# Optimization experiments

Hardware: AMD Instinct MI355X
Metric: run time of the kernel (lower is better)

Reference implementation:

```python
import jax, jax.numpy as jnp
import numpy as np

EMB = 1024
HEADS = 16
HEAD_DIM = EMB // HEADS


def setup_inputs() -> dict:
    key = jax.random.key(0)
    ks = jax.random.split(key, 9)
    B, T = 2, 2048
    s = 1.0 / np.sqrt(EMB)
    x = jax.random.normal(ks[0], (B, T, EMB), dtype=jnp.float32)
    Wq = jax.random.normal(ks[1], (EMB, EMB), dtype=jnp.float32) * s
    bq = jnp.zeros((EMB,), dtype=jnp.float32)
    Wk = jax.random.normal(ks[2], (EMB, EMB), dtype=jnp.float32) * s
    bk = jnp.zeros((EMB,), dtype=jnp.float32)
    Wv = jax.random.normal(ks[3], (EMB, EMB), dtype=jnp.float32) * s
    bv = jnp.zeros((EMB,), dtype=jnp.float32)
    Wo = jax.random.normal(ks[4], (EMB, EMB), dtype=jnp.float32) * s
    bo = jnp.zeros((EMB,), dtype=jnp.float32)
    return {"x": x, "Wq": Wq, "bq": bq, "Wk": Wk, "bk": bk,
            "Wv": Wv, "bv": bv, "Wo": Wo, "bo": bo}


def reference(x, Wq, bq, Wk, bk, Wv, bv, Wo, bo):
    B, T, C = x.shape
    H, D = HEADS, HEAD_DIM
    # QKV projections -> (B, H, T, D)
    q = (x @ Wq + bq).reshape(B, T, H, D).transpose(0, 2, 1, 3)
    k = (x @ Wk + bk).reshape(B, T, H, D).transpose(0, 2, 1, 3)
    v = (x @ Wv + bv).reshape(B, T, H, D).transpose(0, 2, 1, 3)
    scores = jnp.einsum('bhqd,bhkd->bhqk', q, k) / np.sqrt(D).astype(np.float32)
    causal = jnp.tril(jnp.ones((T, T), dtype=bool))  # True where allowed
    scores = jnp.where(causal, scores, -jnp.inf)
    weights = jax.nn.softmax(scores, axis=-1)  # dropout is identity at eval
    out = jnp.einsum('bhqk,bhkd->bhqd', weights, v)
    out = out.transpose(0, 2, 1, 3).reshape(B, T, C)
    return out @ Wo + bo
```

## Files before the change

kernel.cpp:

```cpp
#include <hip/hip_runtime.h>

typedef unsigned short u16;
typedef u16 u16x8 __attribute__((ext_vector_type(8)));
typedef __bf16 bf16x8 __attribute__((ext_vector_type(8)));
typedef float f32x4 __attribute__((ext_vector_type(4)));

#define EMB 1024
#define TT 2048
#define BB 2
#define NHEADS 16
#define HD 64
#define MTOT (BB * TT)

__device__ __forceinline__ u16 f2bf(float f) {
  unsigned u = __builtin_bit_cast(unsigned, f);
  u += 0x7fffu + ((u >> 16) & 1u);
  return (u16)(u >> 16);
}

__device__ __forceinline__ bf16x8 asbf(u16x8 v) {
  return __builtin_bit_cast(bf16x8, v);
}

__device__ __forceinline__ void gload16(const void* g, void* l) {
  __builtin_amdgcn_global_load_lds(
      (const __attribute__((address_space(1))) void*)g,
      (__attribute__((address_space(3))) void*)l, 16, 0, 0);
}

__global__ __launch_bounds__(256) void k_conv_x(const float* __restrict__ x,
                                                u16* __restrict__ xb) {
  int i = blockIdx.x * 256 + threadIdx.x;
  float4 a = ((const float4*)x)[i * 2];
  float4 b = ((const float4*)x)[i * 2 + 1];
  u16x8 o;
  o[0] = f2bf(a.x); o[1] = f2bf(a.y); o[2] = f2bf(a.z); o[3] = f2bf(a.w);
  o[4] = f2bf(b.x); o[5] = f2bf(b.y); o[6] = f2bf(b.z); o[7] = f2bf(b.w);
  ((u16x8*)xb)[i] = o;
}

__global__ __launch_bounds__(256) void k_conv_wT4(
    const float* __restrict__ W0, const float* __restrict__ W1,
    const float* __restrict__ W2, const float* __restrict__ W3,
    u16* __restrict__ T0, u16* __restrict__ T1, u16* __restrict__ T2,
    u16* __restrict__ T3) {
  const int z = blockIdx.z;
  const float* __restrict__ W = (z == 0) ? W0 : (z == 1) ? W1 : (z == 2) ? W2 : W3;
  u16* __restrict__ Wt = (z == 0) ? T0 : (z == 1) ? T1 : (z == 2) ? T2 : T3;
  __shared__ float tile[32][33];
  int bx = blockIdx.x * 32, by = blockIdx.y * 32;
  int tx = threadIdx.x & 31;
  int ty = threadIdx.x >> 5;
#pragma unroll
  for (int r = ty; r < 32; r += 8) tile[r][tx] = W[(by + r) * EMB + bx + tx];
  __syncthreads();
#pragma unroll
  for (int r = ty; r < 32; r += 8)
    Wt[(bx + r) * EMB + by + tx] = f2bf(tile[tx][r]);
}

__global__ __launch_bounds__(256) void k_gemm_qkv(
    const u16* __restrict__ xb, const u16* __restrict__ WqT,
    const u16* __restrict__ WkT, const u16* __restrict__ WvT,
    const float* __restrict__ bq, const float* __restrict__ bk,
    const float* __restrict__ bv, u16* __restrict__ Q, u16* __restrict__ K,
    u16* __restrict__ Vt) {
  __shared__ u16 Al[128 * 32];
  __shared__ u16 Bl[128 * 32];
  const int tid = threadIdx.x;
  const int lane = tid & 63;
  const int w = tid >> 6;
  const int wr = w >> 1, wc = w & 1;
  const int lr = lane & 15, lg = lane >> 4;
  const int m0 = blockIdx.x * 128;
  const int nb = blockIdx.y;
  const int seg = nb >> 3;
  const int n0 = (nb & 7) * 128;
  const u16* __restrict__ Bt = (seg == 0) ? WqT : (seg == 1) ? WkT : WvT;
  const float* __restrict__ bias = (seg == 0) ? bq : (seg == 1) ? bk : bv;

  f32x4 acc[4][4];
#pragma unroll
  for (int i = 0; i < 4; i++)
#pragma unroll
    for (int j = 0; j < 4; j++) acc[i][j] = (f32x4){0.f, 0.f, 0.f, 0.f};

  const int srow = tid >> 2;
  const int scol = (tid & 3) * 8;
  const u16* ga0 = xb + (m0 + srow) * EMB + scol;
  const u16* gb0 = Bt + (n0 + srow) * EMB + scol;
  char* la0 = (char*)Al + w * 1024;
  char* lb0 = (char*)Bl + w * 1024;

  for (int k0 = 0; k0 < EMB; k0 += 32) {
    gload16(ga0 + k0, la0);
    gload16(ga0 + 64 * EMB + k0, la0 + 4096);
    gload16(gb0 + k0, lb0);
    gload16(gb0 + 64 * EMB + k0, lb0 + 4096);
    __syncthreads();
    u16x8 af[4], bfr[4];
#pragma unroll
    for (int mi = 0; mi < 4; mi++)
      af[mi] = *(const u16x8*)&Al[(wr * 64 + mi * 16 + lr) * 32 + lg * 8];
#pragma unroll
    for (int ni = 0; ni < 4; ni++)
      bfr[ni] = *(const u16x8*)&Bl[(wc * 64 + ni * 16 + lr) * 32 + lg * 8];
#pragma unroll
    for (int mi = 0; mi < 4; mi++)
#pragma unroll
      for (int ni = 0; ni < 4; ni++)
        acc[mi][ni] = __builtin_amdgcn_mfma_f32_16x16x32_bf16(
            asbf(af[mi]), asbf(bfr[ni]), acc[mi][ni], 0, 0, 0);
    __syncthreads();
  }

#pragma unroll
  for (int mi = 0; mi < 4; mi++) {
    const int lmb = wr * 64 + mi * 16 + lg * 4;
#pragma unroll
    for (int ni = 0; ni < 4; ni++) {
      const int ln = wc * 64 + ni * 16 + lr;
      const int n = n0 + ln;
      const float bv_ = bias[n];
      const int h = n >> 6, d = n & 63;
#pragma unroll
      for (int r = 0; r < 4; r++) {
        const int m = m0 + lmb + r;
        const int b = m >> 11, t = m & 2047;
        float v = acc[mi][ni][r] + bv_;
        if (seg == 0) {
          v *= 0.125f;
          Q[(((b * NHEADS + h) * TT) + t) * HD + d] = f2bf(v);
        } else if (seg == 1) {
          K[(((b * NHEADS + h) * TT) + t) * HD + d] = f2bf(v);
        } else {
          Vt[(((b * NHEADS + h) * HD) + d) * TT + t] = f2bf(v);
        }
      }
    }
  }
}

__global__ __launch_bounds__(512) void k_attn(const u16* __restrict__ Q,
                                              const u16* __restrict__ Kg,
                                              const u16* __restrict__ Vt,
                                              u16* __restrict__ AO) {
  __shared__ u16 Kl[2][64 * 64];
  __shared__ u16 Vl[2][64 * 64];
  __shared__ u16 Plds[8][16][68];
  const int tid = threadIdx.x;
  const int lane = tid & 63;
  const int w = tid >> 6;
  const int lr = lane & 15, lg = lane >> 4;
  const int bh = blockIdx.x;
  const int pair = blockIdx.y;
  const int lo = pair, hi = 31 - pair;
  const int qblk = (w < 4) ? hi : lo;
  const int myend = qblk;
  const int q0 = qblk * 64 + (w & 3) * 16;
  const u16* __restrict__ Qh = Q + bh * TT * HD;
  const u16* __restrict__ Kh = Kg + bh * TT * HD;
  const u16* __restrict__ Vh = Vt + bh * HD * TT;

  const int srow = tid >> 3;
  const int sc = (tid & 7) ^ (srow & 7);

  u16x8 qf[2];
  qf[0] = *(const u16x8*)&Qh[(q0 + lr) * HD + lg * 8];
  qf[1] = *(const u16x8*)&Qh[(q0 + lr) * HD + 32 + lg * 8];

  f32x4 accO[4];
#pragma unroll
  for (int i = 0; i < 4; i++) accO[i] = (f32x4){0.f, 0.f, 0.f, 0.f};
  float mst[4] = {-__builtin_inff(), -__builtin_inff(), -__builtin_inff(),
                  -__builtin_inff()};
  float lsum[4] = {0.f, 0.f, 0.f, 0.f};

  const int nkt = hi + 1;

  gload16(Kh + srow * HD + sc * 8, (char*)Kl[0] + w * 1024);
  gload16(Vh + srow * TT + 0 + sc * 8, (char*)Vl[0] + w * 1024);
  __syncthreads();

  for (int kt = 0; kt < nkt; ++kt) {
    const int k0 = kt * 64;
    const int cur = kt & 1;
    if (kt + 1 < nkt) {
      const int kn = k0 + 64;
      gload16(Kh + (kn + srow) * HD + sc * 8, (char*)Kl[cur ^ 1] + w * 1024);
      gload16(Vh + srow * TT + kn + sc * 8, (char*)Vl[cur ^ 1] + w * 1024);
    }
    if (kt <= myend) {
      const char* Kc = (const char*)Kl[cur];
      const char* Vc = (const char*)Vl[cur];

      f32x4 s[4];
#pragma unroll
      for (int n = 0; n < 4; n++) s[n] = (f32x4){0.f, 0.f, 0.f, 0.f};
      __builtin_amdgcn_s_setprio(1);
#pragma unroll
      for (int n = 0; n < 4; n++) {
        const int row = n * 16 + lr;
#pragma unroll
        for (int dh = 0; dh < 2; dh++) {
          const int bo = (dh * 64 + lg * 16) ^ ((row & 7) << 4);
          u16x8 kf = *(const u16x8*)(Kc + row * 128 + bo);
          s[n] = __builtin_amdgcn_mfma_f32_16x16x32_bf16(asbf(qf[dh]),
                                                         asbf(kf), s[n], 0, 0, 0);
        }
      }
      __builtin_amdgcn_s_setprio(0);
      if (kt == myend) {
#pragma unroll
        for (int n = 0; n < 4; n++)
#pragma unroll
          for (int r = 0; r < 4; r++) {
            int col = k0 + n * 16 + lr, row = q0 + lg * 4 + r;
            if (col > row) s[n][r] = -__builtin_inff();
          }
      }
      float lmax[4];
#pragma unroll
      for (int r = 0; r < 4; r++)
        lmax[r] = fmaxf(fmaxf(s[0][r], s[1][r]), fmaxf(s[2][r], s[3][r]));
      float g0 = fmaxf(lmax[0] - mst[0], lmax[1] - mst[1]);
      float g1 = fmaxf(lmax[2] - mst[2], lmax[3] - mst[3]);
      if (!__all(fmaxf(g0, g1) <= 8.0f)) {
#pragma unroll
        for (int r = 0; r < 4; r++) {
          float rm = lmax[r];
          rm = fmaxf(rm, __shfl_xor(rm, 1, 16));
          rm = fmaxf(rm, __shfl_xor(rm, 2, 16));
          rm = fmaxf(rm, __shfl_xor(rm, 4, 16));
          rm = fmaxf(rm, __shfl_xor(rm, 8, 16));
          float mnew = fmaxf(mst[r], rm);
          float corr = __expf(mst[r] - mnew);
          lsum[r] *= corr;
          mst[r] = mnew;
#pragma unroll
          for (int dt = 0; dt < 4; dt++) accO[dt][r] *= corr;
        }
      }
#pragma unroll
      for (int r = 0; r < 4; r++) {
        float p0 = __expf(s[0][r] - mst[r]);
        float p1 = __expf(s[1][r] - mst[r]);
        float p2 = __expf(s[2][r] - mst[r]);
        float p3 = __expf(s[3][r] - mst[r]);
        lsum[r] += (p0 + p1) + (p2 + p3);
        const int row = lg * 4 + r;
        Plds[w][row][lr] = f2bf(p0);
        Plds[w][row][16 + lr] = f2bf(p1);
        Plds[w][row][32 + lr] = f2bf(p2);
        Plds[w][row][48 + lr] = f2bf(p3);
      }
      u16x8 pa0 = *(const u16x8*)&Plds[w][lr][lg * 8];
      u16x8 pa1 = *(const u16x8*)&Plds[w][lr][32 + lg * 8];
      __builtin_amdgcn_s_setprio(1);
#pragma unroll
      for (int dt = 0; dt < 4; dt++) {
        const int row = dt * 16 + lr;
        const int bo0 = (lg * 16) ^ ((row & 7) << 4);
        const int bo1 = (64 + lg * 16) ^ ((row & 7) << 4);
        u16x8 vf0 = *(const u16x8*)(Vc + row * 128 + bo0);
        u16x8 vf1 = *(const u16x8*)(Vc + row * 128 + bo1);
        accO[dt] = __builtin_amdgcn_mfma_f32_16x16x32_bf16(asbf(pa0),
                                                           asbf(vf0), accO[dt], 0, 0, 0);
        accO[dt] = __builtin_amdgcn_mfma_f32_16x16x32_bf16(asbf(pa1),
                                                           asbf(vf1), accO[dt], 0, 0, 0);
      }
      __builtin_amdgcn_s_setprio(0);
    }
    __syncthreads();
  }
  float rinv[4];
#pragma unroll
  for (int r = 0; r < 4; r++) {
    float t = lsum[r];
    t += __shfl_xor(t, 1, 16);
    t += __shfl_xor(t, 2, 16);
    t += __shfl_xor(t, 4, 16);
    t += __shfl_xor(t, 8, 16);
    rinv[r] = 1.0f / t;
  }
  const int b = bh >> 4, h = bh & 15;
#pragma unroll
  for (int dt = 0; dt < 4; dt++)
#pragma unroll
    for (int r = 0; r < 4; r++) {
      const int row = q0 + lg * 4 + r;
      const int d = h * 64 + dt * 16 + lr;
      AO[(b * TT + row) * EMB + d] = f2bf(accO[dt][r] * rinv[r]);
    }
}

__global__ __launch_bounds__(256) void k_gemm_out(const u16* __restrict__ AO,
                                                  const u16* __restrict__ WoT,
                                                  const float* __restrict__ bo,
                                                  float* __restrict__ out) {
  __shared__ u16 Al[128 * 32];
  __shared__ u16 Bl[128 * 32];
  const int tid = threadIdx.x;
  const int lane = tid & 63;
  const int w = tid >> 6;
  const int wr = w >> 1, wc = w & 1;
  const int lr = lane & 15, lg = lane >> 4;
  const int m0 = blockIdx.x * 128;
  const int n0 = blockIdx.y * 128;

  f32x4 acc[4][4];
#pragma unroll
  for (int i = 0; i < 4; i++)
#pragma unroll
    for (int j = 0; j < 4; j++) acc[i][j] = (f32x4){0.f, 0.f, 0.f, 0.f};

  const int srow = tid >> 2;
  const int scol = (tid & 3) * 8;
  const u16* ga0 = AO + (m0 + srow) * EMB + scol;
  const u16* gb0 = WoT + (n0 + srow) * EMB + scol;
  char* la0 = (char*)Al + w * 1024;
  char* lb0 = (char*)Bl + w * 1024;

  for (int k0 = 0; k0 < EMB; k0 += 32) {
    gload16(ga0 + k0, la0);
    gload16(ga0 + 64 * EMB + k0, la0 + 4096);
    gload16(gb0 + k0, lb0);
    gload16(gb0 + 64 * EMB + k0, lb0 + 4096);
    __syncthreads();
    u16x8 af[4], bfr[4];
#pragma unroll
    for (int mi = 0; mi < 4; mi++)
      af[mi] = *(const u16x8*)&Al[(wr * 64 + mi * 16 + lr) * 32 + lg * 8];
#pragma unroll
    for (int ni = 0; ni < 4; ni++)
      bfr[ni] = *(const u16x8*)&Bl[(wc * 64 + ni * 16 + lr) * 32 + lg * 8];
#pragma unroll
    for (int mi = 0; mi < 4; mi++)
#pragma unroll
      for (int ni = 0; ni < 4; ni++)
        acc[mi][ni] = __builtin_amdgcn_mfma_f32_16x16x32_bf16(
            asbf(af[mi]), asbf(bfr[ni]), acc[mi][ni], 0, 0, 0);
    __syncthreads();
  }

#pragma unroll
  for (int mi = 0; mi < 4; mi++) {
    const int lmb = wr * 64 + mi * 16 + lg * 4;
#pragma unroll
    for (int ni = 0; ni < 4; ni++) {
      const int ln = wc * 64 + ni * 16 + lr;
      const int n = n0 + ln;
      const float bv_ = bo[n];
#pragma unroll
      for (int r = 0; r < 4; r++) {
        const int m = m0 + lmb + r;
        out[m * EMB + n] = acc[mi][ni][r] + bv_;
      }
    }
  }
}

extern "C" void kernel_launch(void* const* d_in, const int* in_sizes, int n_in,
                              void* d_out, int out_size, void* d_ws,
                              size_t ws_size, hipStream_t stream) {
  const float* x = (const float*)d_in[0];
  const float* Wq = (const float*)d_in[1];
  const float* bq = (const float*)d_in[2];
  const float* Wk = (const float*)d_in[3];
  const float* bk = (const float*)d_in[4];
  const float* Wv = (const float*)d_in[5];
  const float* bv = (const float*)d_in[6];
  const float* Wo = (const float*)d_in[7];
  const float* bo = (const float*)d_in[8];
  float* out = (float*)d_out;

  char* ws = (char*)d_ws;
  u16* xb = (u16*)ws;
  u16* WqT = (u16*)(ws + (8u << 20));
  u16* WkT = (u16*)(ws + (10u << 20));
  u16* WvT = (u16*)(ws + (12u << 20));
  u16* WoT = (u16*)(ws + (14u << 20));
  u16* Qb = (u16*)(ws + (16u << 20));
  u16* Kb = (u16*)(ws + (24u << 20));
  u16* Vtb = (u16*)(ws + (32u << 20));
  u16* AO = xb;

  k_conv_x<<<2048, 256, 0, stream>>>(x, xb);
  dim3 tg(32, 32, 4);
  k_conv_wT4<<<tg, 256, 0, stream>>>(Wq, Wk, Wv, Wo, WqT, WkT, WvT, WoT);
  k_gemm_qkv<<<dim3(32, 24), 256, 0, stream>>>(xb, WqT, WkT, WvT, bq, bk, bv,
                                               Qb, Kb, Vtb);
  k_attn<<<dim3(32, 16), 512, 0, stream>>>(Qb, Kb, Vtb, AO);
  k_gemm_out<<<dim3(32, 8), 256, 0, stream>>>(AO, WoT, bo, out);
}
```

Measured before the change: 122.5 us.

## Double attention KV tile to 128, use exp2 softmax, fuse prep kernels

The attention kernel now processes 128 keys per tile instead of 64, which halves the number of loop iterations and barriers. The pipelining and causal masking are adjusted to the new tile size, and the V tile is split into two 64-wide P·V passes. Q is pre-scaled by log2(e)/8 so the softmax can use exp2f in place of __expf, and the lazy-rescale threshold is raised to match. The x conversion and weight-transpose kernels are merged into one launch, and the manual bf16 rounding is replaced by the hardware conversion. The larger tiles increase LDS and register use, and more wasted work is done on the diagonal tile.

```diff
diff --git a/kernel.cpp b/kernel.cpp
--- a/kernel.cpp
+++ b/kernel.cpp
@@ -12,10 +12,8 @@
 #define HD 64
 #define MTOT (BB * TT)
 
-__device__ __forceinline__ u16 f2bf(float f) {
-  unsigned u = __builtin_bit_cast(unsigned, f);
-  u += 0x7fffu + ((u >> 16) & 1u);
-  return (u16)(u >> 16);
+__device__ __forceinline__ u16 cvt(float f) {
+  return __builtin_bit_cast(u16, (__bf16)f);
 }
 
 __device__ __forceinline__ bf16x8 asbf(u16x8 v) {
@@ -28,35 +26,38 @@
       (__attribute__((address_space(3))) void*)l, 16, 0, 0);
 }
 
-__global__ __launch_bounds__(256) void k_conv_x(const float* __restrict__ x,
-                                                u16* __restrict__ xb) {
-  int i = blockIdx.x * 256 + threadIdx.x;
-  float4 a = ((const float4*)x)[i * 2];
-  float4 b = ((const float4*)x)[i * 2 + 1];
-  u16x8 o;
-  o[0] = f2bf(a.x); o[1] = f2bf(a.y); o[2] = f2bf(a.z); o[3] = f2bf(a.w);
-  o[4] = f2bf(b.x); o[5] = f2bf(b.y); o[6] = f2bf(b.z); o[7] = f2bf(b.w);
-  ((u16x8*)xb)[i] = o;
-}
-
-__global__ __launch_bounds__(256) void k_conv_wT4(
+__global__ __launch_bounds__(256) void k_prep(
+    const float* __restrict__ x, u16* __restrict__ xb,
     const float* __restrict__ W0, const float* __restrict__ W1,
     const float* __restrict__ W2, const float* __restrict__ W3,
     u16* __restrict__ T0, u16* __restrict__ T1, u16* __restrict__ T2,
     u16* __restrict__ T3) {
-  const int z = blockIdx.z;
+  __shared__ float tile[32][33];
+  const int bid = blockIdx.x;
+  const int tid = threadIdx.x;
+  if (bid >= 4096) {
+    int i = (bid - 4096) * 256 + tid;
+    float4 a = ((const float4*)x)[i * 2];
+    float4 b = ((const float4*)x)[i * 2 + 1];
+    u16x8 o;
+    o[0] = cvt(a.x); o[1] = cvt(a.y); o[2] = cvt(a.z); o[3] = cvt(a.w);
+    o[4] = cvt(b.x); o[5] = cvt(b.y); o[6] = cvt(b.z); o[7] = cvt(b.w);
+    ((u16x8*)xb)[i] = o;
+    return;
+  }
+  const int z = bid >> 10;
   const float* __restrict__ W = (z == 0) ? W0 : (z == 1) ? W1 : (z == 2) ? W2 : W3;
   u16* __restrict__ Wt = (z == 0) ? T0 : (z == 1) ? T1 : (z == 2) ? T2 : T3;
-  __shared__ float tile[32][33];
-  int bx = blockIdx.x * 32, by = blockIdx.y * 32;
-  int tx = threadIdx.x & 31;
-  int ty = threadIdx.x >> 5;
+  const int b = bid & 1023;
+  const int bx = (b & 31) * 32, by = (b >> 5) * 32;
+  const int tx = tid & 31;
+  const int ty = tid >> 5;
 #pragma unroll
   for (int r = ty; r < 32; r += 8) tile[r][tx] = W[(by + r) * EMB + bx + tx];
   __syncthreads();
 #pragma unroll
   for (int r = ty; r < 32; r += 8)
-    Wt[(bx + r) * EMB + by + tx] = f2bf(tile[tx][r]);
+    Wt[(bx + r) * EMB + by + tx] = cvt(tile[tx][r]);
 }
 
 __global__ __launch_bounds__(256) void k_gemm_qkv(
@@ -129,12 +130,12 @@
         const int b = m >> 11, t = m & 2047;
         float v = acc[mi][ni][r] + bv_;
         if (seg == 0) {
-          v *= 0.125f;
-          Q[(((b * NHEADS + h) * TT) + t) * HD + d] = f2bf(v);
+          v *= 0.18033688011f;
+          Q[(((b * NHEADS + h) * TT) + t) * HD + d] = cvt(v);
         } else if (seg == 1) {
-          K[(((b * NHEADS + h) * TT) + t) * HD + d] = f2bf(v);
+          K[(((b * NHEADS + h) * TT) + t) * HD + d] = cvt(v);
         } else {
-          Vt[(((b * NHEADS + h) * HD) + d) * TT + t] = f2bf(v);
+          Vt[(((b * NHEADS + h) * HD) + d) * TT + t] = cvt(v);
         }
       }
     }
@@ -145,8 +146,8 @@
                                               const u16* __restrict__ Kg,
                                               const u16* __restrict__ Vt,
                                               u16* __restrict__ AO) {
-  __shared__ u16 Kl[2][64 * 64];
-  __shared__ u16 Vl[2][64 * 64];
+  __shared__ u16 Kl[2][128 * 64];
+  __shared__ u16 Vl[2][64 * 128];
   __shared__ u16 Plds[8][16][68];
   const int tid = threadIdx.x;
   const int lane = tid & 63;
@@ -156,14 +157,16 @@
   const int pair = blockIdx.y;
   const int lo = pair, hi = 31 - pair;
   const int qblk = (w < 4) ? hi : lo;
-  const int myend = qblk;
+  const int myend = qblk >> 1;
   const int q0 = qblk * 64 + (w & 3) * 16;
   const u16* __restrict__ Qh = Q + bh * TT * HD;
   const u16* __restrict__ Kh = Kg + bh * TT * HD;
   const u16* __restrict__ Vh = Vt + bh * HD * TT;
 
-  const int srow = tid >> 3;
-  const int sc = (tid & 7) ^ (srow & 7);
+  const int krow = tid >> 3;
+  const int ksc = (tid & 7) ^ (krow & 7);
+  const int vrow = tid >> 4;
+  const int vgc = (tid & 15) ^ (vrow & 7);
 
   u16x8 qf[2];
   qf[0] = *(const u16x8*)&Qh[(q0 + lr) * HD + lg * 8];
@@ -176,34 +179,44 @@
                   -__builtin_inff()};
   float lsum[4] = {0.f, 0.f, 0.f, 0.f};
 
-  const int nkt = hi + 1;
-
-  gload16(Kh + srow * HD + sc * 8, (char*)Kl[0] + w * 1024);
-  gload16(Vh + srow * TT + 0 + sc * 8, (char*)Vl[0] + w * 1024);
+  const int nkt = (hi >> 1) + 1;
+
+#pragma unroll
+  for (int h = 0; h < 2; h++) {
+    gload16(Kh + (h * 64 + krow) * HD + ksc * 8,
+            (char*)Kl[0] + h * 8192 + w * 1024);
+    gload16(Vh + (h * 32 + vrow) * TT + 0 + vgc * 8,
+            (char*)Vl[0] + h * 8192 + w * 1024);
+  }
   __syncthreads();
 
   for (int kt = 0; kt < nkt; ++kt) {
-    const int k0 = kt * 64;
+    const int k0 = kt * 128;
     const int cur = kt & 1;
     if (kt + 1 < nkt) {
-      const int kn = k0 + 64;
-      gload16(Kh + (kn + srow) * HD + sc * 8, (char*)Kl[cur ^ 1] + w * 1024);
-      gload16(Vh + srow * TT + kn + sc * 8, (char*)Vl[cur ^ 1] + w * 1024);
+      const int kn = k0 + 128;
+#pragma unroll
+      for (int h = 0; h < 2; h++) {
+        gload16(Kh + (kn + h * 64 + krow) * HD + ksc * 8,
+                (char*)Kl[cur ^ 1] + h * 8192 + w * 1024);
+        gload16(Vh + (h * 32 + vrow) * TT + kn + vgc * 8,
+                (char*)Vl[cur ^ 1] + h * 8192 + w * 1024);
+      }
     }
     if (kt <= myend) {
       const char* Kc = (const char*)Kl[cur];
       const char* Vc = (const char*)Vl[cur];
 
-      f32x4 s[4];
-#pragma unroll
-      for (int n = 0; n < 4; n++) s[n] = (f32x4){0.f, 0.f, 0.f, 0.f};
+      f32x4 s[8];
+#pragma unroll
+      for (int n = 0; n < 8; n++) s[n] = (f32x4){0.f, 0.f, 0.f, 0.f};
       __builtin_amdgcn_s_setprio(1);
 #pragma unroll
-      for (int n = 0; n < 4; n++) {
+      for (int n = 0; n < 8; n++) {
         const int row = n * 16 + lr;
 #pragma unroll
         for (int dh = 0; dh < 2; dh++) {
-          const int bo = (dh * 64 + lg * 16) ^ ((row & 7) << 4);
+          const int bo = ((dh * 4 + lg) ^ (lr & 7)) * 16;
           u16x8 kf = *(const u16x8*)(Kc + row * 128 + bo);
           s[n] = __builtin_amdgcn_mfma_f32_16x16x32_bf16(asbf(qf[dh]),
                                                          asbf(kf), s[n], 0, 0, 0);
@@ -212,7 +225,7 @@
       __builtin_amdgcn_s_setprio(0);
       if (kt == myend) {
 #pragma unroll
-        for (int n = 0; n < 4; n++)
+        for (int n = 0; n < 8; n++)
 #pragma unroll
           for (int r = 0; r < 4; r++) {
             int col = k0 + n * 16 + lr, row = q0 + lg * 4 + r;
@@ -221,11 +234,14 @@
       }
       float lmax[4];
 #pragma unroll
-      for (int r = 0; r < 4; r++)
-        lmax[r] = fmaxf(fmaxf(s[0][r], s[1][r]), fmaxf(s[2][r], s[3][r]));
+      for (int r = 0; r < 4; r++) {
+        float a = fmaxf(fmaxf(s[0][r], s[1][r]), fmaxf(s[2][r], s[3][r]));
+        float b = fmaxf(fmaxf(s[4][r], s[5][r]), fmaxf(s[6][r], s[7][r]));
+        lmax[r] = fmaxf(a, b);
+      }
       float g0 = fmaxf(lmax[0] - mst[0], lmax[1] - mst[1]);
       float g1 = fmaxf(lmax[2] - mst[2], lmax[3] - mst[3]);
-      if (!__all(fmaxf(g0, g1) <= 8.0f)) {
+      if (!__all(fmaxf(g0, g1) <= 11.0f)) {
 #pragma unroll
         for (int r = 0; r < 4; r++) {
           float rm = lmax[r];
@@ -234,7 +250,7 @@
           rm = fmaxf(rm, __shfl_xor(rm, 4, 16));
           rm = fmaxf(rm, __shfl_xor(rm, 8, 16));
           float mnew = fmaxf(mst[r], rm);
-          float corr = __expf(mst[r] - mnew);
+          float corr = exp2f(mst[r] - mnew);
           lsum[r] *= corr;
           mst[r] = mnew;
 #pragma unroll
@@ -242,34 +258,37 @@
         }
       }
 #pragma unroll
-      for (int r = 0; r < 4; r++) {
-        float p0 = __expf(s[0][r] - mst[r]);
-        float p1 = __expf(s[1][r] - mst[r]);
-        float p2 = __expf(s[2][r] - mst[r]);
-        float p3 = __expf(s[3][r] - mst[r]);
-        lsum[r] += (p0 + p1) + (p2 + p3);
-        const int row = lg * 4 + r;
-        Plds[w][row][lr] = f2bf(p0);
-        Plds[w][row][16 + lr] = f2bf(p1);
-        Plds[w][row][32 + lr] = f2bf(p2);
-        Plds[w][row][48 + lr] = f2bf(p3);
-      }
-      u16x8 pa0 = *(const u16x8*)&Plds[w][lr][lg * 8];
-      u16x8 pa1 = *(const u16x8*)&Plds[w][lr][32 + lg * 8];
-      __builtin_amdgcn_s_setprio(1);
-#pragma unroll
-      for (int dt = 0; dt < 4; dt++) {
-        const int row = dt * 16 + lr;
-        const int bo0 = (lg * 16) ^ ((row & 7) << 4);
-        const int bo1 = (64 + lg * 16) ^ ((row & 7) << 4);
-        u16x8 vf0 = *(const u16x8*)(Vc + row * 128 + bo0);
-        u16x8 vf1 = *(const u16x8*)(Vc + row * 128 + bo1);
-        accO[dt] = __builtin_amdgcn_mfma_f32_16x16x32_bf16(asbf(pa0),
-                                                           asbf(vf0), accO[dt], 0, 0, 0);
-        accO[dt] = __builtin_amdgcn_mfma_f32_16x16x32_bf16(asbf(pa1),
-                                                           asbf(vf1), accO[dt], 0, 0, 0);
-      }
-      __builtin_amdgcn_s_setprio(0);
+      for (int p64 = 0; p64 < 2; p64++) {
+#pragma unroll
+        for (int r = 0; r < 4; r++) {
+          float p0 = exp2f(s[p64 * 4 + 0][r] - mst[r]);
+          float p1 = exp2f(s[p64 * 4 + 1][r] - mst[r]);
+          float p2 = exp2f(s[p64 * 4 + 2][r] - mst[r]);
+          float p3 = exp2f(s[p64 * 4 + 3][r] - mst[r]);
+          lsum[r] += (p0 + p1) + (p2 + p3);
+          const int row = lg * 4 + r;
+          Plds[w][row][lr] = cvt(p0);
+          Plds[w][row][16 + lr] = cvt(p1);
+          Plds[w][row][32 + lr] = cvt(p2);
+          Plds[w][row][48 + lr] = cvt(p3);
+        }
+        u16x8 pa0 = *(const u16x8*)&Plds[w][lr][lg * 8];
+        u16x8 pa1 = *(const u16x8*)&Plds[w][lr][32 + lg * 8];
+        __builtin_amdgcn_s_setprio(1);
+#pragma unroll
+        for (int dt = 0; dt < 4; dt++) {
+          const int row = dt * 16 + lr;
+          const int bo0 = p64 * 128 + ((lg ^ (lr & 7)) * 16);
+          const int bo1 = p64 * 128 + (((4 + lg) ^ (lr & 7)) * 16);
+          u16x8 vf0 = *(const u16x8*)(Vc + row * 256 + bo0);
+          u16x8 vf1 = *(const u16x8*)(Vc + row * 256 + bo1);
+          accO[dt] = __builtin_amdgcn_mfma_f32_16x16x32_bf16(
+              asbf(pa0), asbf(vf0), accO[dt], 0, 0, 0);
+          accO[dt] = __builtin_amdgcn_mfma_f32_16x16x32_bf16(
+              asbf(pa1), asbf(vf1), accO[dt], 0, 0, 0);
+        }
+        __builtin_amdgcn_s_setprio(0);
+      }
     }
     __syncthreads();
   }
@@ -290,7 +309,7 @@
     for (int r = 0; r < 4; r++) {
       const int row = q0 + lg * 4 + r;
       const int d = h * 64 + dt * 16 + lr;
-      AO[(b * TT + row) * EMB + d] = f2bf(accO[dt][r] * rinv[r]);
+      AO[(b * TT + row) * EMB + d] = cvt(accO[dt][r] * rinv[r]);
     }
 }
 
@@ -385,9 +404,7 @@
   u16* Vtb = (u16*)(ws + (32u << 20));
   u16* AO = xb;
 
-  k_conv_x<<<2048, 256, 0, stream>>>(x, xb);
-  dim3 tg(32, 32, 4);
-  k_conv_wT4<<<tg, 256, 0, stream>>>(Wq, Wk, Wv, Wo, WqT, WkT, WvT, WoT);
+  k_prep<<<6144, 256, 0, stream>>>(x, xb, Wq, Wk, Wv, Wo, WqT, WkT, WvT, WoT);
   k_gemm_qkv<<<dim3(32, 24), 256, 0, stream>>>(xb, WqT, WkT, WvT, bq, bk, bv,
                                                Qb, Kb, Vtb);
   k_attn<<<dim3(32, 16), 512, 0, stream>>>(Qb, Kb, Vtb, AO);
```

After: 136.7 us. +11.6%, slower.

## Fuse prep kernels, swizzle GEMM tiles, use exp2 softmax and hardware bf16 cvt

Applied to the files above, without the earlier changes.

Merges the x conversion and the weight transpose into a single prep launch to save one kernel launch. Remaps GEMM workgroup IDs with an XCD-style swizzle so that neighbouring tiles share cache. Folds log2(e) into the Q scale so softmax can use exp2f directly, and raises the lazy-rescale threshold to 11, which is about 8 in natural-log units. Replaces the manual round-to-nearest bf16 conversion with the compiler's native conversion.

```diff
diff --git a/kernel.cpp b/kernel.cpp
--- a/kernel.cpp
+++ b/kernel.cpp
@@ -12,10 +12,8 @@
 #define HD 64
 #define MTOT (BB * TT)
 
-__device__ __forceinline__ u16 f2bf(float f) {
-  unsigned u = __builtin_bit_cast(unsigned, f);
-  u += 0x7fffu + ((u >> 16) & 1u);
-  return (u16)(u >> 16);
+__device__ __forceinline__ u16 cvt(float f) {
+  return __builtin_bit_cast(u16, (__bf16)f);
 }
 
 __device__ __forceinline__ bf16x8 asbf(u16x8 v) {
@@ -28,35 +26,38 @@
       (__attribute__((address_space(3))) void*)l, 16, 0, 0);
 }
 
-__global__ __launch_bounds__(256) void k_conv_x(const float* __restrict__ x,
-                                                u16* __restrict__ xb) {
-  int i = blockIdx.x * 256 + threadIdx.x;
-  float4 a = ((const float4*)x)[i * 2];
-  float4 b = ((const float4*)x)[i * 2 + 1];
-  u16x8 o;
-  o[0] = f2bf(a.x); o[1] = f2bf(a.y); o[2] = f2bf(a.z); o[3] = f2bf(a.w);
-  o[4] = f2bf(b.x); o[5] = f2bf(b.y); o[6] = f2bf(b.z); o[7] = f2bf(b.w);
-  ((u16x8*)xb)[i] = o;
-}
-
-__global__ __launch_bounds__(256) void k_conv_wT4(
+__global__ __launch_bounds__(256) void k_prep(
+    const float* __restrict__ x, u16* __restrict__ xb,
     const float* __restrict__ W0, const float* __restrict__ W1,
     const float* __restrict__ W2, const float* __restrict__ W3,
     u16* __restrict__ T0, u16* __restrict__ T1, u16* __restrict__ T2,
     u16* __restrict__ T3) {
-  const int z = blockIdx.z;
+  __shared__ float tile[32][33];
+  const int bid = blockIdx.x;
+  const int tid = threadIdx.x;
+  if (bid >= 4096) {
+    int i = (bid - 4096) * 256 + tid;
+    float4 a = ((const float4*)x)[i * 2];
+    float4 b = ((const float4*)x)[i * 2 + 1];
+    u16x8 o;
+    o[0] = cvt(a.x); o[1] = cvt(a.y); o[2] = cvt(a.z); o[3] = cvt(a.w);
+    o[4] = cvt(b.x); o[5] = cvt(b.y); o[6] = cvt(b.z); o[7] = cvt(b.w);
+    ((u16x8*)xb)[i] = o;
+    return;
+  }
+  const int z = bid >> 10;
   const float* __restrict__ W = (z == 0) ? W0 : (z == 1) ? W1 : (z == 2) ? W2 : W3;
   u16* __restrict__ Wt = (z == 0) ? T0 : (z == 1) ? T1 : (z == 2) ? T2 : T3;
-  __shared__ float tile[32][33];
-  int bx = blockIdx.x * 32, by = blockIdx.y * 32;
-  int tx = threadIdx.x & 31;
-  int ty = threadIdx.x >> 5;
+  const int b = bid & 1023;
+  const int bx = (b & 31) * 32, by = (b >> 5) * 32;
+  const int tx = tid & 31;
+  const int ty = tid >> 5;
 #pragma unroll
   for (int r = ty; r < 32; r += 8) tile[r][tx] = W[(by + r) * EMB + bx + tx];
   __syncthreads();
 #pragma unroll
   for (int r = ty; r < 32; r += 8)
-    Wt[(bx + r) * EMB + by + tx] = f2bf(tile[tx][r]);
+    Wt[(bx + r) * EMB + by + tx] = cvt(tile[tx][r]);
 }
 
 __global__ __launch_bounds__(256) void k_gemm_qkv(
@@ -72,8 +73,10 @@
   const int w = tid >> 6;
   const int wr = w >> 1, wc = w & 1;
   const int lr = lane & 15, lg = lane >> 4;
-  const int m0 = blockIdx.x * 128;
-  const int nb = blockIdx.y;
+  const int wg = blockIdx.y * 32 + blockIdx.x;
+  const int swz = (wg & 7) * 96 + (wg >> 3);
+  const int m0 = (swz & 31) * 128;
+  const int nb = swz >> 5;
   const int seg = nb >> 3;
   const int n0 = (nb & 7) * 128;
   const u16* __restrict__ Bt = (seg == 0) ? WqT : (seg == 1) ? WkT : WvT;
@@ -129,12 +132,12 @@
         const int b = m >> 11, t = m & 2047;
         float v = acc[mi][ni][r] + bv_;
         if (seg == 0) {
-          v *= 0.125f;
-          Q[(((b * NHEADS + h) * TT) + t) * HD + d] = f2bf(v);
+          v *= 0.18033688011f;
+          Q[(((b * NHEADS + h) * TT) + t) * HD + d] = cvt(v);
         } else if (seg == 1) {
-          K[(((b * NHEADS + h) * TT) + t) * HD + d] = f2bf(v);
+          K[(((b * NHEADS + h) * TT) + t) * HD + d] = cvt(v);
         } else {
-          Vt[(((b * NHEADS + h) * HD) + d) * TT + t] = f2bf(v);
+          Vt[(((b * NHEADS + h) * HD) + d) * TT + t] = cvt(v);
         }
       }
     }
@@ -225,7 +228,7 @@
         lmax[r] = fmaxf(fmaxf(s[0][r], s[1][r]), fmaxf(s[2][r], s[3][r]));
       float g0 = fmaxf(lmax[0] - mst[0], lmax[1] - mst[1]);
       float g1 = fmaxf(lmax[2] - mst[2], lmax[3] - mst[3]);
-      if (!__all(fmaxf(g0, g1) <= 8.0f)) {
+      if (!__all(fmaxf(g0, g1) <= 11.0f)) {
 #pragma unroll
         for (int r = 0; r < 4; r++) {
           float rm = lmax[r];
@@ -234,7 +237,7 @@
           rm = fmaxf(rm, __shfl_xor(rm, 4, 16));
           rm = fmaxf(rm, __shfl_xor(rm, 8, 16));
           float mnew = fmaxf(mst[r], rm);
-          float corr = __expf(mst[r] - mnew);
+          float corr = exp2f(mst[r] - mnew);
           lsum[r] *= corr;
           mst[r] = mnew;
 #pragma unroll
@@ -243,16 +246,16 @@
       }
 #pragma unroll
       for (int r = 0; r < 4; r++) {
-        float p0 = __expf(s[0][r] - mst[r]);
-        float p1 = __expf(s[1][r] - mst[r]);
-        float p2 = __expf(s[2][r] - mst[r]);
-        float p3 = __expf(s[3][r] - mst[r]);
+        float p0 = exp2f(s[0][r] - mst[r]);
+        float p1 = exp2f(s[1][r] - mst[r]);
+        float p2 = exp2f(s[2][r] - mst[r]);
+        float p3 = exp2f(s[3][r] - mst[r]);
         lsum[r] += (p0 + p1) + (p2 + p3);
         const int row = lg * 4 + r;
-        Plds[w][row][lr] = f2bf(p0);
-        Plds[w][row][16 + lr] = f2bf(p1);
-        Plds[w][row][32 + lr] = f2bf(p2);
-        Plds[w][row][48 + lr] = f2bf(p3);
+        Plds[w][row][lr] = cvt(p0);
+        Plds[w][row][16 + lr] = cvt(p1);
+        Plds[w][row][32 + lr] = cvt(p2);
+        Plds[w][row][48 + lr] = cvt(p3);
       }
       u16x8 pa0 = *(const u16x8*)&Plds[w][lr][lg * 8];
       u16x8 pa1 = *(const u16x8*)&Plds[w][lr][32 + lg * 8];
@@ -290,7 +293,7 @@
     for (int r = 0; r < 4; r++) {
       const int row = q0 + lg * 4 + r;
       const int d = h * 64 + dt * 16 + lr;
-      AO[(b * TT + row) * EMB + d] = f2bf(accO[dt][r] * rinv[r]);
+      AO[(b * TT + row) * EMB + d] = cvt(accO[dt][r] * rinv[r]);
     }
 }
 
@@ -305,8 +308,10 @@
   const int w = tid >> 6;
   const int wr = w >> 1, wc = w & 1;
   const int lr = lane & 15, lg = lane >> 4;
-  const int m0 = blockIdx.x * 128;
-  const int n0 = blockIdx.y * 128;
+  const int wg = blockIdx.y * 32 + blockIdx.x;
+  const int swz = (wg & 7) * 32 + (wg >> 3);
+  const int m0 = (swz & 31) * 128;
+  const int n0 = (swz >> 5) * 128;
 
   f32x4 acc[4][4];
 #pragma unroll
@@ -385,9 +390,7 @@
   u16* Vtb = (u16*)(ws + (32u << 20));
   u16* AO = xb;
 
-  k_conv_x<<<2048, 256, 0, stream>>>(x, xb);
-  dim3 tg(32, 32, 4);
-  k_conv_wT4<<<tg, 256, 0, stream>>>(Wq, Wk, Wv, Wo, WqT, WkT, WvT, WoT);
+  k_prep<<<6144, 256, 0, stream>>>(x, xb, Wq, Wk, Wv, Wo, WqT, WkT, WvT, WoT);
   k_gemm_qkv<<<dim3(32, 24), 256, 0, stream>>>(xb, WqT, WkT, WvT, bq, bk, bv,
                                                Qb, Kb, Vtb);
   k_attn<<<dim3(32, 16), 512, 0, stream>>>(Qb, Kb, Vtb, AO);
```

New measurement: 136.4 us. 1.11x slower.
